# Kernel tuning notes

Hardware: AMD Instinct MI355X
Metric: run time of the kernel (lower is better)

## Reference

```python
import jax, jax.numpy as jnp
import numpy as np

B, S, D, H = 2, 2048, 1024, 16
HD = D // H  # head_dim = 64
ROPE_BASE = 10000.0
INIT_STD = 0.02


def setup_inputs() -> dict:
    key = jax.random.key(0)
    k1, k2, k3 = jax.random.split(key, 3)
    x = jax.random.normal(k1, (B, S, D), dtype=jnp.float32)
    w_qkv = jax.random.normal(k2, (3 * D, D), dtype=jnp.float32) * INIT_STD
    w_out = jax.random.normal(k3, (D, D), dtype=jnp.float32) * (1.0 / np.sqrt(D))
    b_out = jnp.zeros((D,), dtype=jnp.float32)
    return {"x": x, "w_qkv": w_qkv, "w_out": w_out, "b_out": b_out}


def _rope_cos_sin(s_len, head_dim, dtype):
    theta = 1.0 / ROPE_BASE ** (jnp.arange(0, head_dim, 2, dtype=jnp.float32) / head_dim)
    freqs = jnp.outer(jnp.arange(s_len, dtype=jnp.float32), theta)  # [s, d/2]
    freqs = jnp.concatenate([freqs, freqs], axis=-1)  # [s, d]
    return jnp.cos(freqs).astype(dtype), jnp.sin(freqs).astype(dtype)


def _apply_rope(qk, cos, sin):
    # qk: [b, h, s, d]; rotate-half: (-x2, x1)
    d2 = qk.shape[-1] // 2
    x1, x2 = qk[..., :d2], qk[..., d2:]
    rot = jnp.concatenate([-x2, x1], axis=-1)
    return qk * cos + rot * sin


def reference(x, w_qkv, w_out, b_out):
    b, s, d = x.shape
    qkv = jnp.einsum('bsd,ed->bse', x, w_qkv)  # [b, s, 3D]
    qkv = qkv.reshape(b, s, 3 * H, HD).transpose(0, 2, 1, 3)  # [b, 3h, s, d]
    qk, v = qkv[:, :2 * H], qkv[:, 2 * H:]
    cos, sin = _rope_cos_sin(s, HD, x.dtype)
    qk = _apply_rope(qk, cos, sin)
    q, k = qk[:, :H], qk[:, H:]
    scale = 1.0 / np.sqrt(HD)
    scores = jnp.einsum('bhqd,bhkd->bhqk', q, k) * scale  # [b, h, s, s]
    causal = jnp.tril(jnp.ones((s, s), dtype=bool))
    scores = jnp.where(causal, scores, jnp.finfo(scores.dtype).min)
    attn = jax.nn.softmax(scores, axis=-1)
    o = jnp.einsum('bhqk,bhkd->bhqd', attn, v)  # [b, h, s, d]
    o = o.transpose(0, 2, 1, 3).reshape(b, s, d)
    return jnp.einsum('bsd,ed->bse', o, w_out) + b_out
```

## Files before the change

### kernel.cpp

```cpp
#include <hip/hip_runtime.h>
#include <hip/hip_fp16.h>
#include <math.h>

#define B_  2
#define S_  2048
#define D_  1024
#define H_  16
#define HD_ 64

typedef _Float16  f16;
typedef __attribute__((ext_vector_type(8))) _Float16 f16x8;
typedef __attribute__((ext_vector_type(4))) _Float16 f16x4;
typedef __attribute__((ext_vector_type(4))) float    f32x4;

#define LOG2E 1.4426950408889634f
#define L2_10000_DIV32 0.41524101186092029f

__device__ __forceinline__ float fin(float v) { return (v == v) ? v : 0.0f; }

__device__ __forceinline__ f16x8 cvt8(const float* p) {
  float4 a = *(const float4*)p;
  float4 b = *(const float4*)(p + 4);
  f16x8 h;
  h[0] = (f16)a.x; h[1] = (f16)a.y; h[2] = (f16)a.z; h[3] = (f16)a.w;
  h[4] = (f16)b.x; h[5] = (f16)b.y; h[6] = (f16)b.z; h[7] = (f16)b.w;
  return h;
}

__device__ __forceinline__ int swz64(int r, int c) {
  return r * 64 + ((((c >> 3) ^ (r & 7)) << 3) | (c & 7));
}

#define GLD16(g, l)                                                        \
  __builtin_amdgcn_global_load_lds(                                        \
      (const __attribute__((address_space(1))) void*)(g),                  \
      (__attribute__((address_space(3))) void*)(l), 16, 0, 0)

__global__ void __launch_bounds__(256)
k_cvt3(const float* __restrict__ wq, const float* __restrict__ wo,
       const float* __restrict__ x,
       f16* __restrict__ wqh, f16* __restrict__ woh, f16* __restrict__ xh,
       float2* __restrict__ tab, int doX)
{
  const int NWQ = 3 * D_ * D_ / 4, NWO = D_ * D_ / 4, NX = B_ * S_ * D_ / 4;
  const int n = NWQ + NWO + (doX ? NX : 0);
  for (int i = blockIdx.x * 256 + threadIdx.x; i < n; i += gridDim.x * 256) {
    const float* src; f16* dst; int j;
    if (i < NWQ)            { src = wq; dst = wqh; j = i; }
    else if (i < NWQ + NWO) { src = wo; dst = woh; j = i - NWQ; }
    else                    { src = x;  dst = xh;  j = i - NWQ - NWO; }
    float4 v = ((const float4*)src)[j];
    f16x4 h = {(f16)v.x, (f16)v.y, (f16)v.z, (f16)v.w};
    ((f16x4*)dst)[j] = h;
  }
  for (int i = blockIdx.x * 256 + threadIdx.x; i < S_ * 32; i += gridDim.x * 256) {
    const int p = i >> 5, j = i & 31;
    const float th = exp2f(-(float)j * L2_10000_DIV32);
    float s, c;
    sincosf((float)p * th, &s, &c);
    tab[i] = make_float2(c, s);
  }
}

template <bool XF16>
__global__ void __launch_bounds__(256)
k_qkv3(const float* __restrict__ xf, const f16* __restrict__ xh,
       const f16* __restrict__ wqh, const float2* __restrict__ tab,
       f16* __restrict__ Qb, f16* __restrict__ Kb, f16* __restrict__ Vt)
{
  __shared__ __align__(16) f16 As[128 * 64];
  __shared__ __align__(16) f16 Bs[128 * 64];
  const int t = threadIdx.x;
  const int w = t >> 6;
  const int lane = t & 63;
  const int ll = lane & 15;
  const int quad = lane >> 4;
  const int wm = w >> 1, wn = w & 1;
  const int row0 = blockIdx.y * 128;
  const int col0 = blockIdx.x * 128;

  const f32x4 fz = {0.f, 0.f, 0.f, 0.f};
  f32x4 acc[4][4];
#pragma unroll
  for (int i = 0; i < 4; ++i)
#pragma unroll
    for (int j = 0; j < 4; ++j) acc[i][j] = fz;

  const int rO = lane >> 3;
  const int gc = (lane & 7) ^ rO;
  const f16* gah2 = xh  + (size_t)(row0 + w * 8 + rO) * D_ + gc * 8;
  const f16* gb2  = wqh + (size_t)(col0 + w * 8 + rO) * D_ + gc * 8;

  const int ldr = t >> 3;
  const int ldk = (t & 7) * 8;
  const float* gaf = xf + (size_t)(row0 + ldr) * D_ + ldk;

  for (int kt = 0; kt < D_; kt += 64) {
    f16x8 ra[4];
    if (!XF16) {
#pragma unroll
      for (int i = 0; i < 4; ++i)
        ra[i] = cvt8(gaf + (size_t)i * 32 * D_ + kt);
    }
    __syncthreads();
    if (XF16) {
#pragma unroll
      for (int i = 0; i < 4; ++i) {
        GLD16(gah2 + (size_t)(i * 32) * D_ + kt, &As[(i * 32 + w * 8) * 64]);
        GLD16(gb2  + (size_t)(i * 32) * D_ + kt, &Bs[(i * 32 + w * 8) * 64]);
      }
    } else {
#pragma unroll
      for (int i = 0; i < 4; ++i) {
        *(f16x8*)&As[swz64(i * 32 + ldr, ldk)] = ra[i];
        GLD16(gb2 + (size_t)(i * 32) * D_ + kt, &Bs[(i * 32 + w * 8) * 64]);
      }
    }
    __syncthreads();
#pragma unroll
    for (int kk = 0; kk < 64; kk += 32) {
      f16x8 a[4], b[4];
#pragma unroll
      for (int mt = 0; mt < 4; ++mt)
        a[mt] = *(const f16x8*)&As[swz64(wm * 64 + mt * 16 + ll, kk + quad * 8)];
#pragma unroll
      for (int nt = 0; nt < 4; ++nt)
        b[nt] = *(const f16x8*)&Bs[swz64(wn * 64 + nt * 16 + ll, kk + quad * 8)];
#pragma unroll
      for (int mt = 0; mt < 4; ++mt)
#pragma unroll
        for (int nt = 0; nt < 4; ++nt)
          acc[mt][nt] = __builtin_amdgcn_mfma_f32_16x16x32_f16(
              a[mt], b[nt], acc[mt][nt], 0, 0, 0);
    }
  }

  const int h3 = (col0 >> 6) + wn;
  if (h3 < 32) {
    f16* dst = (h3 < 16) ? Qb : Kb;
    const int h = (h3 < 16) ? h3 : h3 - 16;
#pragma unroll
    for (int mt = 0; mt < 4; ++mt) {
#pragma unroll
      for (int r = 0; r < 4; ++r) {
        const int row = row0 + wm * 64 + mt * 16 + quad * 4 + r;
        const int b = row >> 11;
        const int p = row & (S_ - 1);
        f16* base = dst + ((size_t)(b * H_ + h) * S_ + p) * HD_;
        const float2 cs0 = tab[p * 32 + ll];
        const float2 cs1 = tab[p * 32 + 16 + ll];
        {
          float x1 = acc[mt][0][r], x2 = acc[mt][2][r];
          base[ll]      = (f16)fin(x1 * cs0.x - x2 * cs0.y);
          base[ll + 32] = (f16)fin(x2 * cs0.x + x1 * cs0.y);
        }
        {
          float x1 = acc[mt][1][r], x2 = acc[mt][3][r];
          base[16 + ll]      = (f16)fin(x1 * cs1.x - x2 * cs1.y);
          base[16 + ll + 32] = (f16)fin(x2 * cs1.x + x1 * cs1.y);
        }
      }
    }
  } else {
    const int hv = h3 - 32;
#pragma unroll
    for (int mt = 0; mt < 4; ++mt)
#pragma unroll
      for (int nt = 0; nt < 4; ++nt)
#pragma unroll
        for (int r = 0; r < 4; ++r) {
          const int row = row0 + wm * 64 + mt * 16 + quad * 4 + r;
          const int b = row >> 11;
          const int p = row & (S_ - 1);
          const int dd = nt * 16 + ll;
          Vt[((size_t)(b * H_ + hv) * HD_ + dd) * S_ + p] = (f16)fin(acc[mt][nt][r]);
        }
  }
}

__device__ __forceinline__ bool softmax_tile4(
    f32x4 sc[4], bool diag, int qloc, int ll, int quad,
    float& mrun, float& lrun, float& alpha, f16* Pt)
{
  if (diag) {
#pragma unroll
    for (int nt = 0; nt < 4; ++nt)
#pragma unroll
      for (int r = 0; r < 4; ++r)
        if ((nt * 16 + quad * 4 + r) > qloc) sc[nt][r] = -3.0e4f;
  }
  float pm = mrun;
#pragma unroll
  for (int nt = 0; nt < 4; ++nt)
#pragma unroll
    for (int r = 0; r < 4; ++r) pm = fmaxf(pm, sc[nt][r]);
  pm = fmaxf(pm, __shfl_xor(pm, 16));
  pm = fmaxf(pm, __shfl_xor(pm, 32));
  const bool resc = !__all(pm <= mrun + 8.0f);
  if (resc) { alpha = exp2f(mrun - pm); mrun = pm; }
  float ps = 0.f;
#pragma unroll
  for (int nt = 0; nt < 4; ++nt) {
    f16x4 pk;
#pragma unroll
    for (int r = 0; r < 4; ++r) {
      float p = exp2f(sc[nt][r] - mrun);
      ps += p;
      pk[r] = (f16)p;
    }
    *(f16x4*)&Pt[swz64(ll, nt * 16 + quad * 4)] = pk;
  }
  ps += __shfl_xor(ps, 16);
  ps += __shfl_xor(ps, 32);
  lrun = (resc ? lrun * alpha : lrun) + ps;
  return resc;
}

__device__ __forceinline__ void write_o4(
    f32x4 acco[4], float lrun, f16* Pt, int ll, int quad, int w,
    int qt, size_t bh, f16* Ob)
{
  const float inv = 1.0f / fmaxf(lrun, 1e-30f);
#pragma unroll
  for (int dg = 0; dg < 4; ++dg) {
    f16x4 ov;
#pragma unroll
    for (int r = 0; r < 4; ++r) ov[r] = (f16)fin(acco[dg][r] * inv);
    *(f16x4*)&Pt[swz64(ll, dg * 16 + quad * 4)] = ov;
  }
#pragma unroll
  for (int s2 = 0; s2 < 2; ++s2) {
    f16x8 o = *(const f16x8*)&Pt[swz64(ll, (quad + 4 * s2) * 8)];
    const size_t row = bh * S_ + qt * 64 + w * 16 + ll;
    *(f16x8*)&Ob[row * HD_ + (quad + 4 * s2) * 8] = o;
  }
}

__global__ void __launch_bounds__(256, 4)
k_attn5(const f16* Qb, const f16* __restrict__ Kb,
        const f16* __restrict__ Vt, f16* Ob)
{
  __shared__ __align__(16) f16 Ks[2][64 * 64];
  __shared__ __align__(16) f16 Ps[4][16 * 64];

  const int t = threadIdx.x;
  const int w = t >> 6;
  const int lane = t & 63;
  const int ll = lane & 15;
  const int quad = lane >> 4;
  const int bx = blockIdx.x;
  const int base = (bx & 1) ? 31 - (bx >> 1) : (bx >> 1);
  const int qt = ((int)blockIdx.y < 8) ? base : 31 - base;
  const int h = blockIdx.y;
  const int b = blockIdx.z;
  const size_t bh = (size_t)b * H_ + h;
  const f16* Qg = Qb + bh * S_ * HD_;
  const f16* Kg = Kb + bh * S_ * HD_;
  const f16* Vg = Vt + bh * HD_ * S_;

  f16x8 bq[2];
  {
    const f16 hsc = (f16)(0.125f * LOG2E);
#pragma unroll
    for (int k2 = 0; k2 < 2; ++k2) {
      bq[k2] = *(const f16x8*)(Qg + (size_t)(qt * 64 + w * 16 + ll) * HD_ + k2 * 32 + quad * 8);
#pragma unroll
      for (int e = 0; e < 8; ++e) bq[k2][e] *= hsc;
    }
  }
  const int sr = t >> 2;
  const int scc = (t & 3) * 16;
  {
    f16x8 a0 = *(const f16x8*)(Kg + (size_t)sr * HD_ + scc);
    f16x8 a1 = *(const f16x8*)(Kg + (size_t)sr * HD_ + scc + 8);
    *(f16x8*)&Ks[0][swz64(sr, scc)]     = a0;
    *(f16x8*)&Ks[0][swz64(sr, scc + 8)] = a1;
  }
  __syncthreads();

  const f32x4 fz = {0.f, 0.f, 0.f, 0.f};
  f32x4 acco[4] = {fz, fz, fz, fz};
  float m = -3.0e4f, l = 0.f;
  const int qloc = w * 16 + ll;
  f16* Pt = &Ps[w][0];

  for (int kt = 0; kt <= qt; ++kt) {
    const int cur = kt & 1;
    const bool pre = (kt < qt);
    f16x8 nk0, nk1;
    if (pre) {
      const int kn = (kt + 1) * 64;
      nk0 = *(const f16x8*)(Kg + (size_t)(kn + sr) * HD_ + scc);
      nk1 = *(const f16x8*)(Kg + (size_t)(kn + sr) * HD_ + scc + 8);
    }
    const f16* Kc = Ks[cur];

    f16x8 av[2][4];
#pragma unroll
    for (int k2 = 0; k2 < 2; ++k2)
#pragma unroll
      for (int dg = 0; dg < 4; ++dg)
        av[k2][dg] = *(const f16x8*)(Vg + (size_t)(dg * 16 + ll) * S_ + kt * 64 + k2 * 32 + quad * 8);

    f16x8 ak[2][4];
#pragma unroll
    for (int k2 = 0; k2 < 2; ++k2)
#pragma unroll
      for (int nt = 0; nt < 4; ++nt)
        ak[k2][nt] = *(const f16x8*)&Kc[swz64(nt * 16 + ll, k2 * 32 + quad * 8)];

    f32x4 s[4] = {fz, fz, fz, fz};
#pragma unroll
    for (int k2 = 0; k2 < 2; ++k2)
#pragma unroll
      for (int nt = 0; nt < 4; ++nt)
        s[nt] = __builtin_amdgcn_mfma_f32_16x16x32_f16(ak[k2][nt], bq[k2], s[nt], 0, 0, 0);

    float alpha;
    const bool resc = softmax_tile4(s, kt == qt, qloc, ll, quad, m, l, alpha, Pt);
    if (resc) {
#pragma unroll
      for (int dg = 0; dg < 4; ++dg)
#pragma unroll
        for (int r = 0; r < 4; ++r) acco[dg][r] *= alpha;
    }
#pragma unroll
    for (int k2 = 0; k2 < 2; ++k2) {
      f16x8 bp = *(const f16x8*)&Pt[swz64(ll, k2 * 32 + quad * 8)];
#pragma unroll
      for (int dg = 0; dg < 4; ++dg)
        acco[dg] = __builtin_amdgcn_mfma_f32_16x16x32_f16(av[k2][dg], bp, acco[dg], 0, 0, 0);
    }

    if (pre) {
      *(f16x8*)&Ks[1 - cur][swz64(sr, scc)]     = nk0;
      *(f16x8*)&Ks[1 - cur][swz64(sr, scc + 8)] = nk1;
    }
    __syncthreads();
  }

  write_o4(acco, l, Pt, ll, quad, w, qt, bh, Ob);
}

__global__ void __launch_bounds__(256)
k_out3(const f16* __restrict__ Ob, const f16* __restrict__ Wh,
       const float* __restrict__ bias, float* __restrict__ out)
{
  __shared__ __align__(16) f16 As[64 * 64];
  __shared__ __align__(16) f16 Bs[128 * 64];
  const int t = threadIdx.x;
  const int w = t >> 6;
  const int lane = t & 63;
  const int ll = lane & 15;
  const int quad = lane >> 4;
  const int wm = w >> 1, wn = w & 1;
  const int row0 = blockIdx.y * 64;
  const int col0 = blockIdx.x * 128;
  const int bb = row0 >> 11;
  const int s0 = row0 & (S_ - 1);

  const f32x4 fz = {0.f, 0.f, 0.f, 0.f};
  f32x4 acc[2][4];
#pragma unroll
  for (int i = 0; i < 2; ++i)
#pragma unroll
    for (int j = 0; j < 4; ++j) acc[i][j] = fz;

  const int rO = lane >> 3;
  const int gc = (lane & 7) ^ rO;
  const f16* gb2 = Wh + (size_t)(col0 + w * 8 + rO) * D_ + gc * 8;

  for (int kt = 0; kt < 16; ++kt) {
    const f16* ga2 = Ob + (((size_t)(bb * H_ + kt)) * S_ + s0 + w * 8 + rO) * HD_ + gc * 8;
    __syncthreads();
#pragma unroll
    for (int i = 0; i < 2; ++i)
      GLD16(ga2 + (size_t)(i * 32) * HD_, &As[(i * 32 + w * 8) * 64]);
#pragma unroll
    for (int i = 0; i < 4; ++i)
      GLD16(gb2 + (size_t)(i * 32) * D_ + kt * 64, &Bs[(i * 32 + w * 8) * 64]);
    __syncthreads();
#pragma unroll
    for (int kk = 0; kk < 64; kk += 32) {
      f16x8 a[2], b[4];
#pragma unroll
      for (int mt = 0; mt < 2; ++mt)
        a[mt] = *(const f16x8*)&As[swz64(wm * 32 + mt * 16 + ll, kk + quad * 8)];
#pragma unroll
      for (int nt = 0; nt < 4; ++nt)
        b[nt] = *(const f16x8*)&Bs[swz64(wn * 64 + nt * 16 + ll, kk + quad * 8)];
#pragma unroll
      for (int mt = 0; mt < 2; ++mt)
#pragma unroll
        for (int nt = 0; nt < 4; ++nt)
          acc[mt][nt] = __builtin_amdgcn_mfma_f32_16x16x32_f16(
              a[mt], b[nt], acc[mt][nt], 0, 0, 0);
    }
  }

#pragma unroll
  for (int mt = 0; mt < 2; ++mt)
#pragma unroll
    for (int r = 0; r < 4; ++r) {
      const int row = row0 + wm * 32 + mt * 16 + quad * 4 + r;
#pragma unroll
      for (int nt = 0; nt < 4; ++nt) {
        const int col = col0 + wn * 64 + nt * 16 + ll;
        out[(size_t)row * D_ + col] = fin(acc[mt][nt][r] + bias[col]);
      }
    }
}

extern "C" void kernel_launch(void* const* d_in, const int* in_sizes, int n_in,
                              void* d_out, int out_size, void* d_ws, size_t ws_size,
                              hipStream_t stream) {
  const float* x    = (const float*)d_in[0];
  const float* wqkv = (const float*)d_in[1];
  const float* wout = (const float*)d_in[2];
  const float* bout = (const float*)d_in[3];
  float* out = (float*)d_out;

  char* ws = (char*)d_ws;
  f16* wqh = (f16*)(ws);
  f16* Qb  = (f16*)(ws + 6291456);
  f16* Kb  = (f16*)(ws + 14680064);
  f16* Vt  = (f16*)(ws + 23068672);
  f16* woh = (f16*)(ws + 31457280);
  const bool bigws = ws_size >= (size_t)41943040;
  f16* xh  = (f16*)(ws + 33554432);
  float2* tab = (float2*)d_out;

  k_cvt3<<<2048, 256, 0, stream>>>(wqkv, wout, x, wqh, woh, xh, tab, bigws ? 1 : 0);
  if (bigws)
    k_qkv3<true><<<dim3(3 * D_ / 128, (B_ * S_) / 128), 256, 0, stream>>>(
        x, xh, wqh, tab, Qb, Kb, Vt);
  else
    k_qkv3<false><<<dim3(3 * D_ / 128, (B_ * S_) / 128), 256, 0, stream>>>(
        x, xh, wqh, tab, Qb, Kb, Vt);
  k_attn5<<<dim3(32, H_, B_), 256, 0, stream>>>(Qb, Kb, Vt, Qb );
  k_out3<<<dim3(D_ / 128, (B_ * S_) / 64), 256, 0, stream>>>(
      Qb, woh, bout, out);
}
```

Before: 210.0 us.

## Split long causal query tiles across two blocks and merge with log-sum-exp

The 16 longest query tiles per head are now split into two halves along the key range and run by separate blocks, so the 32 causal tiles become 48 more evenly sized work items. A new merge kernel combines the two fp16 partial outputs using per-row log-sum-exp values, with scratch space taken from the output buffer. V tiles are now double-buffered in shared memory like K, replacing direct global loads, and s_setprio is raised around the MFMA sections. The cost is an extra kernel launch, a partial-output round trip through memory, and more LDS per block, which may lower occupancy.

New measurement: 193.2 us. 1.09x faster.

```diff
diff --git a/kernel.cpp b/kernel.cpp
--- a/kernel.cpp
+++ b/kernel.cpp
@@ -217,8 +217,7 @@
 }
 
 __device__ __forceinline__ void write_o4(
-    f32x4 acco[4], float lrun, f16* Pt, int ll, int quad, int w,
-    int qt, size_t bh, f16* Ob)
+    f32x4 acco[4], float lrun, f16* Pt, int ll, int quad, int w, f16* dst)
 {
   const float inv = 1.0f / fmaxf(lrun, 1e-30f);
 #pragma unroll
@@ -231,16 +230,17 @@
 #pragma unroll
   for (int s2 = 0; s2 < 2; ++s2) {
     f16x8 o = *(const f16x8*)&Pt[swz64(ll, (quad + 4 * s2) * 8)];
-    const size_t row = bh * S_ + qt * 64 + w * 16 + ll;
-    *(f16x8*)&Ob[row * HD_ + (quad + 4 * s2) * 8] = o;
+    *(f16x8*)&dst[(size_t)(w * 16 + ll) * HD_ + (quad + 4 * s2) * 8] = o;
   }
 }
 
 __global__ void __launch_bounds__(256, 4)
-k_attn5(const f16* Qb, const f16* __restrict__ Kb,
-        const f16* __restrict__ Vt, f16* Ob)
+k_attn6(const f16* Qb, const f16* __restrict__ Kb,
+        const f16* __restrict__ Vt, f16* Ob,
+        f16* __restrict__ Opart, float* __restrict__ Lbuf)
 {
   __shared__ __align__(16) f16 Ks[2][64 * 64];
+  __shared__ __align__(16) f16 Vs[2][64 * 64];
   __shared__ __align__(16) f16 Ps[4][16 * 64];
 
   const int t = threadIdx.x;
@@ -248,15 +248,28 @@
   const int lane = t & 63;
   const int ll = lane & 15;
   const int quad = lane >> 4;
-  const int bx = blockIdx.x;
-  const int base = (bx & 1) ? 31 - (bx >> 1) : (bx >> 1);
-  const int qt = ((int)blockIdx.y < 8) ? base : 31 - base;
+
+  const int px = blockIdx.x;
+  int qt, kt0, kt1, half;
+  bool split;
+  if (px < 32) {
+    qt = 31 - (px >> 1);
+    half = px & 1;
+    split = true;
+    const int mid = (qt + 1) >> 1;
+    kt0 = half ? mid : 0;
+    kt1 = half ? qt + 1 : mid;
+  } else {
+    qt = 47 - px;
+    half = 0; split = false;
+    kt0 = 0; kt1 = qt + 1;
+  }
   const int h = blockIdx.y;
   const int b = blockIdx.z;
-  const size_t bh = (size_t)b * H_ + h;
-  const f16* Qg = Qb + bh * S_ * HD_;
-  const f16* Kg = Kb + bh * S_ * HD_;
-  const f16* Vg = Vt + bh * HD_ * S_;
+  const int bh = b * H_ + h;
+  const f16* Qg = Qb + (size_t)bh * S_ * HD_;
+  const f16* Kg = Kb + (size_t)bh * S_ * HD_;
+  const f16* Vg = Vt + (size_t)bh * HD_ * S_;
 
   f16x8 bq[2];
   {
@@ -271,10 +284,14 @@
   const int sr = t >> 2;
   const int scc = (t & 3) * 16;
   {
-    f16x8 a0 = *(const f16x8*)(Kg + (size_t)sr * HD_ + scc);
-    f16x8 a1 = *(const f16x8*)(Kg + (size_t)sr * HD_ + scc + 8);
+    f16x8 a0 = *(const f16x8*)(Kg + (size_t)(kt0 * 64 + sr) * HD_ + scc);
+    f16x8 a1 = *(const f16x8*)(Kg + (size_t)(kt0 * 64 + sr) * HD_ + scc + 8);
+    f16x8 b0 = *(const f16x8*)(Vg + (size_t)sr * S_ + kt0 * 64 + scc);
+    f16x8 b1 = *(const f16x8*)(Vg + (size_t)sr * S_ + kt0 * 64 + scc + 8);
     *(f16x8*)&Ks[0][swz64(sr, scc)]     = a0;
     *(f16x8*)&Ks[0][swz64(sr, scc + 8)] = a1;
+    *(f16x8*)&Vs[0][swz64(sr, scc)]     = b0;
+    *(f16x8*)&Vs[0][swz64(sr, scc + 8)] = b1;
   }
   __syncthreads();
 
@@ -284,23 +301,19 @@
   const int qloc = w * 16 + ll;
   f16* Pt = &Ps[w][0];
 
-  for (int kt = 0; kt <= qt; ++kt) {
-    const int cur = kt & 1;
-    const bool pre = (kt < qt);
-    f16x8 nk0, nk1;
+  for (int kt = kt0; kt < kt1; ++kt) {
+    const int cur = (kt - kt0) & 1;
+    const bool pre = (kt + 1 < kt1);
+    f16x8 nk0, nk1, nv0, nv1;
     if (pre) {
       const int kn = (kt + 1) * 64;
       nk0 = *(const f16x8*)(Kg + (size_t)(kn + sr) * HD_ + scc);
       nk1 = *(const f16x8*)(Kg + (size_t)(kn + sr) * HD_ + scc + 8);
+      nv0 = *(const f16x8*)(Vg + (size_t)sr * S_ + kn + scc);
+      nv1 = *(const f16x8*)(Vg + (size_t)sr * S_ + kn + scc + 8);
     }
     const f16* Kc = Ks[cur];
-
-    f16x8 av[2][4];
-#pragma unroll
-    for (int k2 = 0; k2 < 2; ++k2)
-#pragma unroll
-      for (int dg = 0; dg < 4; ++dg)
-        av[k2][dg] = *(const f16x8*)(Vg + (size_t)(dg * 16 + ll) * S_ + kt * 64 + k2 * 32 + quad * 8);
+    const f16* Vc = Vs[cur];
 
     f16x8 ak[2][4];
 #pragma unroll
@@ -310,11 +323,20 @@
         ak[k2][nt] = *(const f16x8*)&Kc[swz64(nt * 16 + ll, k2 * 32 + quad * 8)];
 
     f32x4 s[4] = {fz, fz, fz, fz};
+    __builtin_amdgcn_s_setprio(1);
 #pragma unroll
     for (int k2 = 0; k2 < 2; ++k2)
 #pragma unroll
       for (int nt = 0; nt < 4; ++nt)
         s[nt] = __builtin_amdgcn_mfma_f32_16x16x32_f16(ak[k2][nt], bq[k2], s[nt], 0, 0, 0);
+    __builtin_amdgcn_s_setprio(0);
+
+    f16x8 av[2][4];
+#pragma unroll
+    for (int k2 = 0; k2 < 2; ++k2)
+#pragma unroll
+      for (int dg = 0; dg < 4; ++dg)
+        av[k2][dg] = *(const f16x8*)&Vc[swz64(dg * 16 + ll, k2 * 32 + quad * 8)];
 
     float alpha;
     const bool resc = softmax_tile4(s, kt == qt, qloc, ll, quad, m, l, alpha, Pt);
@@ -324,6 +346,7 @@
 #pragma unroll
         for (int r = 0; r < 4; ++r) acco[dg][r] *= alpha;
     }
+    __builtin_amdgcn_s_setprio(1);
 #pragma unroll
     for (int k2 = 0; k2 < 2; ++k2) {
       f16x8 bp = *(const f16x8*)&Pt[swz64(ll, k2 * 32 + quad * 8)];
@@ -331,15 +354,55 @@
       for (int dg = 0; dg < 4; ++dg)
         acco[dg] = __builtin_amdgcn_mfma_f32_16x16x32_f16(av[k2][dg], bp, acco[dg], 0, 0, 0);
     }
+    __builtin_amdgcn_s_setprio(0);
 
     if (pre) {
       *(f16x8*)&Ks[1 - cur][swz64(sr, scc)]     = nk0;
       *(f16x8*)&Ks[1 - cur][swz64(sr, scc + 8)] = nk1;
+      *(f16x8*)&Vs[1 - cur][swz64(sr, scc)]     = nv0;
+      *(f16x8*)&Vs[1 - cur][swz64(sr, scc + 8)] = nv1;
     }
     __syncthreads();
   }
 
-  write_o4(acco, l, Pt, ll, quad, w, qt, bh, Ob);
+  if (!split) {
+    write_o4(acco, l, Pt, ll, quad, w, Ob + ((size_t)bh * S_ + qt * 64) * HD_);
+  } else {
+    const int pp = (bh * 16 + (qt - 16)) * 2 + half;
+    if (quad == 0)
+      Lbuf[pp * 64 + w * 16 + ll] = m + log2f(fmaxf(l, 1e-30f));
+    write_o4(acco, l, Pt, ll, quad, w, Opart + (size_t)pp * 4096);
+  }
+}
+
+__global__ void __launch_bounds__(256)
+k_mrg(const f16* __restrict__ Opart, const float* __restrict__ Lbuf,
+      f16* __restrict__ Ob)
+{
+  const int t = threadIdx.x;
+  const int qt = 16 + blockIdx.x;
+  const int bh = blockIdx.z * H_ + blockIdx.y;
+  const int pp0 = (bh * 16 + (qt - 16)) * 2;
+  const int row = t >> 2;
+  const int cs = (t & 3) * 16;
+  const float L0 = Lbuf[pp0 * 64 + row];
+  const float L1 = Lbuf[(pp0 + 1) * 64 + row];
+  const float M = fmaxf(L0, L1);
+  const float w0 = exp2f(L0 - M), w1 = exp2f(L1 - M);
+  const float inv = 1.0f / (w0 + w1);
+  const f16x8 a0 = *(const f16x8*)&Opart[(size_t)pp0 * 4096 + row * 64 + cs];
+  const f16x8 a1 = *(const f16x8*)&Opart[(size_t)pp0 * 4096 + row * 64 + cs + 8];
+  const f16x8 b0 = *(const f16x8*)&Opart[(size_t)(pp0 + 1) * 4096 + row * 64 + cs];
+  const f16x8 b1 = *(const f16x8*)&Opart[(size_t)(pp0 + 1) * 4096 + row * 64 + cs + 8];
+  f16x8 o0, o1;
+#pragma unroll
+  for (int e = 0; e < 8; ++e) {
+    o0[e] = (f16)fin(((float)a0[e] * w0 + (float)b0[e] * w1) * inv);
+    o1[e] = (f16)fin(((float)a1[e] * w0 + (float)b1[e] * w1) * inv);
+  }
+  f16* dst = Ob + ((size_t)bh * S_ + qt * 64 + row) * HD_ + cs;
+  *(f16x8*)dst = o0;
+  *(f16x8*)(dst + 8) = o1;
 }
 
 __global__ void __launch_bounds__(256)
@@ -428,7 +491,11 @@
   f16* woh = (f16*)(ws + 31457280);
   const bool bigws = ws_size >= (size_t)41943040;
   f16* xh  = (f16*)(ws + 33554432);
-  float2* tab = (float2*)d_out;
+
+  char* od = (char*)d_out;
+  f16*    Opart = (f16*)od;
+  float*  Lbuf  = (float*)(od + 8388608);
+  float2* tab   = (float2*)(od + 9437184);
 
   k_cvt3<<<2048, 256, 0, stream>>>(wqkv, wout, x, wqh, woh, xh, tab, bigws ? 1 : 0);
   if (bigws)
@@ -437,7 +504,9 @@
   else
     k_qkv3<false><<<dim3(3 * D_ / 128, (B_ * S_) / 128), 256, 0, stream>>>(
         x, xh, wqh, tab, Qb, Kb, Vt);
-  k_attn5<<<dim3(32, H_, B_), 256, 0, stream>>>(Qb, Kb, Vt, Qb );
+  k_attn6<<<dim3(48, H_, B_), 256, 0, stream>>>(Qb, Kb, Vt, Qb ,
+                                                Opart, Lbuf);
+  k_mrg<<<dim3(16, H_, B_), 256, 0, stream>>>(Opart, Lbuf, Qb);
   k_out3<<<dim3(D_ / 128, (B_ * S_) / 64), 256, 0, stream>>>(
       Qb, woh, bout, out);
 }
```

## Stage V tiles in shared memory with double buffering and unrolled loop

Applied to the files above, without the earlier changes.

The attention kernel now stages V tiles in double-buffered shared memory alongside K, instead of loading V fragments directly from global memory inside the loop. The loop is manually unrolled by two through a macro, with precomputed LDS pointers for the swizzled addresses. s_setprio is raised around the MFMA blocks. The rope table scratch location in the output buffer also moves. The aim is to hide global-load latency for V and cut address arithmetic, at the cost of more shared memory per block, which may lower occupancy.

Result: faster. 182.5 us (-13.1%).

```diff
diff --git a/kernel.cpp b/kernel.cpp
--- a/kernel.cpp
+++ b/kernel.cpp
@@ -178,9 +178,9 @@
   }
 }
 
-__device__ __forceinline__ bool softmax_tile4(
-    f32x4 sc[4], bool diag, int qloc, int ll, int quad,
-    float& mrun, float& lrun, float& alpha, f16* Pt)
+__device__ __forceinline__ bool softmax_tile7(
+    f32x4 sc[4], bool diag, int qloc, int quad,
+    float& mrun, float& lrun, float& alpha, f16* const pst[4])
 {
   if (diag) {
 #pragma unroll
@@ -208,7 +208,7 @@
       ps += p;
       pk[r] = (f16)p;
     }
-    *(f16x4*)&Pt[swz64(ll, nt * 16 + quad * 4)] = pk;
+    *(f16x4*)pst[nt] = pk;
   }
   ps += __shfl_xor(ps, 16);
   ps += __shfl_xor(ps, 32);
@@ -216,9 +216,10 @@
   return resc;
 }
 
-__device__ __forceinline__ void write_o4(
-    f32x4 acco[4], float lrun, f16* Pt, int ll, int quad, int w,
-    int qt, size_t bh, f16* Ob)
+__device__ __forceinline__ void write_o7(
+    f32x4 acco[4], float lrun, f16* const pst[4],
+    const f16* pb0, const f16* pb1,
+    int ll, int quad, int w, int qt, size_t bh, f16* Ob)
 {
   const float inv = 1.0f / fmaxf(lrun, 1e-30f);
 #pragma unroll
@@ -226,21 +227,84 @@
     f16x4 ov;
 #pragma unroll
     for (int r = 0; r < 4; ++r) ov[r] = (f16)fin(acco[dg][r] * inv);
-    *(f16x4*)&Pt[swz64(ll, dg * 16 + quad * 4)] = ov;
-  }
-#pragma unroll
-  for (int s2 = 0; s2 < 2; ++s2) {
-    f16x8 o = *(const f16x8*)&Pt[swz64(ll, (quad + 4 * s2) * 8)];
-    const size_t row = bh * S_ + qt * 64 + w * 16 + ll;
-    *(f16x8*)&Ob[row * HD_ + (quad + 4 * s2) * 8] = o;
-  }
-}
+    *(f16x4*)pst[dg] = ov;
+  }
+  const size_t row = bh * S_ + qt * 64 + w * 16 + ll;
+  f16x8 o0 = *(const f16x8*)pb0;
+  f16x8 o1 = *(const f16x8*)pb1;
+  *(f16x8*)&Ob[row * HD_ + quad * 8]      = o0;
+  *(f16x8*)&Ob[row * HD_ + 32 + quad * 8] = o1;
+}
+
+#define ABODY(KB0, KB1, VB0, VB1, WKA, WKB, WVA, WVB, PRE, DIAG)           \
+  do {                                                                     \
+    f16x8 nk0, nk1, nv0, nv1;                                              \
+    if (PRE) {                                                             \
+      nk0 = *(const f16x8*)pK; nk1 = *(const f16x8*)(pK + 8);              \
+    }                                                                      \
+    f16x8 ak[2][4];                                                        \
+    _Pragma("unroll")                                                      \
+    for (int nt = 0; nt < 4; ++nt) {                                       \
+      ak[0][nt] = *(const f16x8*)(KB0 + nt * 1024);                        \
+      ak[1][nt] = *(const f16x8*)(KB1 + nt * 1024);                        \
+    }                                                                      \
+    f32x4 s[4] = {fz, fz, fz, fz};                                         \
+    __builtin_amdgcn_s_setprio(1);                                         \
+    _Pragma("unroll")                                                      \
+    for (int k2 = 0; k2 < 2; ++k2)                                         \
+      _Pragma("unroll")                                                    \
+      for (int nt = 0; nt < 4; ++nt)                                       \
+        s[nt] = __builtin_amdgcn_mfma_f32_16x16x32_f16(                    \
+            ak[k2][nt], bq[k2], s[nt], 0, 0, 0);                           \
+    __builtin_amdgcn_s_setprio(0);                                         \
+    if (PRE) {                                                             \
+      nv0 = *(const f16x8*)pV; nv1 = *(const f16x8*)(pV + 8);              \
+      pK += 64 * HD_; pV += 64;                                            \
+    }                                                                      \
+    float alpha;                                                           \
+    const bool resc = softmax_tile7(s, DIAG, qloc, quad, m, l, alpha, pst);\
+    if (resc) {                                                            \
+      _Pragma("unroll")                                                    \
+      for (int dg = 0; dg < 4; ++dg)                                       \
+        _Pragma("unroll")                                                  \
+        for (int r = 0; r < 4; ++r) acco[dg][r] *= alpha;                  \
+    }                                                                      \
+    f16x8 av[2][4];                                                        \
+    _Pragma("unroll")                                                      \
+    for (int dg = 0; dg < 4; ++dg) {                                       \
+      av[0][dg] = *(const f16x8*)(VB0 + dg * 1024);                        \
+      av[1][dg] = *(const f16x8*)(VB1 + dg * 1024);                        \
+    }                                                                      \
+    f16x8 bp0 = *(const f16x8*)pb0;                                        \
+    f16x8 bp1 = *(const f16x8*)pb1;                                        \
+    __builtin_amdgcn_s_setprio(1);                                         \
+    _Pragma("unroll")                                                      \
+    for (int dg = 0; dg < 4; ++dg)                                         \
+      acco[dg] = __builtin_amdgcn_mfma_f32_16x16x32_f16(                   \
+          av[0][dg], bp0, acco[dg], 0, 0, 0);                              \
+    _Pragma("unroll")                                                      \
+    for (int dg = 0; dg < 4; ++dg)                                         \
+      acco[dg] = __builtin_amdgcn_mfma_f32_16x16x32_f16(                   \
+          av[1][dg], bp1, acco[dg], 0, 0, 0);                              \
+    __builtin_amdgcn_s_setprio(0);                                         \
+    if (PRE) {                                                             \
+      *(f16x8*)WKA = nk0; *(f16x8*)WKB = nk1;                              \
+      *(f16x8*)WVA = nv0; *(f16x8*)WVB = nv1;                              \
+    }                                                                      \
+    __syncthreads();                                                       \
+  } while (0)
+
+#define ABODY_B0(PRE, DIAG) \
+  ABODY(kb00, kb01, vb00, vb01, wk1a, wk1b, wv1a, wv1b, PRE, DIAG)
+#define ABODY_B1(PRE, DIAG) \
+  ABODY(kb10, kb11, vb10, vb11, wk0a, wk0b, wv0a, wv0b, PRE, DIAG)
 
 __global__ void __launch_bounds__(256, 4)
-k_attn5(const f16* Qb, const f16* __restrict__ Kb,
+k_attn7(const f16* Qb, const f16* __restrict__ Kb,
         const f16* __restrict__ Vt, f16* Ob)
 {
   __shared__ __align__(16) f16 Ks[2][64 * 64];
+  __shared__ __align__(16) f16 Vs[2][64 * 64];
   __shared__ __align__(16) f16 Ps[4][16 * 64];
 
   const int t = threadIdx.x;
@@ -268,78 +332,68 @@
       for (int e = 0; e < 8; ++e) bq[k2][e] *= hsc;
     }
   }
+
+  f16* Pt = &Ps[w][0];
+  const f16* kb00 = &Ks[0][swz64(ll, quad * 8)];
+  const f16* kb01 = &Ks[0][swz64(ll, 32 + quad * 8)];
+  const f16* kb10 = &Ks[1][swz64(ll, quad * 8)];
+  const f16* kb11 = &Ks[1][swz64(ll, 32 + quad * 8)];
+  const f16* vb00 = &Vs[0][swz64(ll, quad * 8)];
+  const f16* vb01 = &Vs[0][swz64(ll, 32 + quad * 8)];
+  const f16* vb10 = &Vs[1][swz64(ll, quad * 8)];
+  const f16* vb11 = &Vs[1][swz64(ll, 32 + quad * 8)];
+  const f16* pb0  = &Pt[swz64(ll, quad * 8)];
+  const f16* pb1  = &Pt[swz64(ll, 32 + quad * 8)];
+  f16* pst[4] = { &Pt[swz64(ll, 0 * 16 + quad * 4)],
+                  &Pt[swz64(ll, 1 * 16 + quad * 4)],
+                  &Pt[swz64(ll, 2 * 16 + quad * 4)],
+                  &Pt[swz64(ll, 3 * 16 + quad * 4)] };
   const int sr = t >> 2;
   const int scc = (t & 3) * 16;
+  f16* wk0a = &Ks[0][swz64(sr, scc)];
+  f16* wk0b = &Ks[0][swz64(sr, scc + 8)];
+  f16* wk1a = &Ks[1][swz64(sr, scc)];
+  f16* wk1b = &Ks[1][swz64(sr, scc + 8)];
+  f16* wv0a = &Vs[0][swz64(sr, scc)];
+  f16* wv0b = &Vs[0][swz64(sr, scc + 8)];
+  f16* wv1a = &Vs[1][swz64(sr, scc)];
+  f16* wv1b = &Vs[1][swz64(sr, scc + 8)];
+
   {
     f16x8 a0 = *(const f16x8*)(Kg + (size_t)sr * HD_ + scc);
     f16x8 a1 = *(const f16x8*)(Kg + (size_t)sr * HD_ + scc + 8);
-    *(f16x8*)&Ks[0][swz64(sr, scc)]     = a0;
-    *(f16x8*)&Ks[0][swz64(sr, scc + 8)] = a1;
+    f16x8 b0 = *(const f16x8*)(Vg + (size_t)sr * S_ + scc);
+    f16x8 b1 = *(const f16x8*)(Vg + (size_t)sr * S_ + scc + 8);
+    *(f16x8*)wk0a = a0;
+    *(f16x8*)wk0b = a1;
+    *(f16x8*)wv0a = b0;
+    *(f16x8*)wv0b = b1;
   }
   __syncthreads();
+
+  const f16* pK = Kg + (size_t)(64 + sr) * HD_ + scc;
+  const f16* pV = Vg + (size_t)sr * S_ + 64 + scc;
 
   const f32x4 fz = {0.f, 0.f, 0.f, 0.f};
   f32x4 acco[4] = {fz, fz, fz, fz};
   float m = -3.0e4f, l = 0.f;
   const int qloc = w * 16 + ll;
-  f16* Pt = &Ps[w][0];
-
-  for (int kt = 0; kt <= qt; ++kt) {
-    const int cur = kt & 1;
-    const bool pre = (kt < qt);
-    f16x8 nk0, nk1;
-    if (pre) {
-      const int kn = (kt + 1) * 64;
-      nk0 = *(const f16x8*)(Kg + (size_t)(kn + sr) * HD_ + scc);
-      nk1 = *(const f16x8*)(Kg + (size_t)(kn + sr) * HD_ + scc + 8);
-    }
-    const f16* Kc = Ks[cur];
-
-    f16x8 av[2][4];
-#pragma unroll
-    for (int k2 = 0; k2 < 2; ++k2)
-#pragma unroll
-      for (int dg = 0; dg < 4; ++dg)
-        av[k2][dg] = *(const f16x8*)(Vg + (size_t)(dg * 16 + ll) * S_ + kt * 64 + k2 * 32 + quad * 8);
-
-    f16x8 ak[2][4];
-#pragma unroll
-    for (int k2 = 0; k2 < 2; ++k2)
-#pragma unroll
-      for (int nt = 0; nt < 4; ++nt)
-        ak[k2][nt] = *(const f16x8*)&Kc[swz64(nt * 16 + ll, k2 * 32 + quad * 8)];
-
-    f32x4 s[4] = {fz, fz, fz, fz};
-#pragma unroll
-    for (int k2 = 0; k2 < 2; ++k2)
-#pragma unroll
-      for (int nt = 0; nt < 4; ++nt)
-        s[nt] = __builtin_amdgcn_mfma_f32_16x16x32_f16(ak[k2][nt], bq[k2], s[nt], 0, 0, 0);
-
-    float alpha;
-    const bool resc = softmax_tile4(s, kt == qt, qloc, ll, quad, m, l, alpha, Pt);
-    if (resc) {
-#pragma unroll
-      for (int dg = 0; dg < 4; ++dg)
-#pragma unroll
-        for (int r = 0; r < 4; ++r) acco[dg][r] *= alpha;
-    }
-#pragma unroll
-    for (int k2 = 0; k2 < 2; ++k2) {
-      f16x8 bp = *(const f16x8*)&Pt[swz64(ll, k2 * 32 + quad * 8)];
-#pragma unroll
-      for (int dg = 0; dg < 4; ++dg)
-        acco[dg] = __builtin_amdgcn_mfma_f32_16x16x32_f16(av[k2][dg], bp, acco[dg], 0, 0, 0);
-    }
-
-    if (pre) {
-      *(f16x8*)&Ks[1 - cur][swz64(sr, scc)]     = nk0;
-      *(f16x8*)&Ks[1 - cur][swz64(sr, scc + 8)] = nk1;
-    }
-    __syncthreads();
-  }
-
-  write_o4(acco, l, Pt, ll, quad, w, qt, bh, Ob);
+
+  int j = 0;
+  while (j + 1 < qt) {
+    ABODY_B0(true, false);
+    ABODY_B1(true, false);
+    j += 2;
+  }
+  if (j < qt) {
+    ABODY_B0(true, false);
+    ++j;
+    ABODY_B1(false, true);
+  } else {
+    ABODY_B0(false, true);
+  }
+
+  write_o7(acco, l, pst, pb0, pb1, ll, quad, w, qt, bh, Ob);
 }
 
 __global__ void __launch_bounds__(256)
@@ -428,7 +482,8 @@
   f16* woh = (f16*)(ws + 31457280);
   const bool bigws = ws_size >= (size_t)41943040;
   f16* xh  = (f16*)(ws + 33554432);
-  float2* tab = (float2*)d_out;
+
+  float2* tab = (float2*)((char*)d_out + 9437184);
 
   k_cvt3<<<2048, 256, 0, stream>>>(wqkv, wout, x, wqh, woh, xh, tab, bigws ? 1 : 0);
   if (bigws)
@@ -437,7 +492,7 @@
   else
     k_qkv3<false><<<dim3(3 * D_ / 128, (B_ * S_) / 128), 256, 0, stream>>>(
         x, xh, wqh, tab, Qb, Kb, Vt);
-  k_attn5<<<dim3(32, H_, B_), 256, 0, stream>>>(Qb, Kb, Vt, Qb );
+  k_attn7<<<dim3(32, H_, B_), 256, 0, stream>>>(Qb, Kb, Vt, Qb );
   k_out3<<<dim3(D_ / 128, (B_ * S_) / 64), 256, 0, stream>>>(
       Qb, woh, bout, out);
 }
```
